# Kernel optimization log

Hardware: AMD Instinct MI355X
Metric: run time of the kernel (lower is better)

The kernel has to match this reference:

```python
import jax, jax.numpy as jnp
import numpy as np

# Dimensions (see shape_source)
B, L, D, H = 2, 2048, 768, 12   # batch, seq_len, hidden, heads (bert-base)
E, T, W = 32, 8, 4               # entities per doc, triggers = first T entities, span width
R, N = 57, 20                    # relation types, NOTA embeddings

# Static (trigger, object) pair index lists: s in [0,T), o in [0,E), s != o  -> P = T*(E-1)
_s = np.repeat(np.arange(T), E)
_o = np.tile(np.arange(E), T)
_keep = _s != _o
S_IDX = jnp.asarray(_s[_keep])   # [P]
O_IDX = jnp.asarray(_o[_keep])   # [P]
P = int(_keep.sum())             # 248


def setup_inputs() -> dict:
    key = jax.random.key(0)
    k1, k2, k3, k4, k5 = jax.random.split(key, 5)
    return {
        "sequence_output": jax.random.normal(k1, (B, L, D), jnp.float32),
        # attention weights are nonnegative (post-softmax) -> uniform fill
        "attention": jax.random.uniform(k2, (B, H, L, L), jnp.float32),
        "relation_embeddings": jax.random.normal(k3, (R, 3 * D), jnp.float32),
        "nota_embeddings": jax.random.normal(k4, (N, 3 * D), jnp.float32),
        "span_starts": jax.random.randint(k5, (B, E), 0, L - W, dtype=jnp.int32),
    }


def reference(sequence_output, attention, relation_embeddings, nota_embeddings, span_starts):
    # Span token indices: [B, E, W]
    idx = span_starts[..., None] + jnp.arange(W)
    b_ix = jnp.arange(B)[:, None, None]

    # Ragged span mean-pooling of token embeddings -> entity embeddings [B, E, D]
    ent_emb = sequence_output[b_ix, idx].mean(axis=2)

    # Mean over span tokens of attention rows -> per-entity attention [B, E, H, L]
    att_t = attention.transpose(0, 2, 1, 3)          # [B, L, H, L]
    ent_att = att_t[b_ix, idx].mean(axis=2)          # [B, E, H, L]

    # Localized context per (trigger s, object o) pair:
    # A = A_s * A_o ; q = sum over heads ; a = q / q.sum() ; c = H^T a
    A = ent_att[:, S_IDX] * ent_att[:, O_IDX]        # [B, P, H, L]
    q = A.sum(axis=2)                                 # [B, P, L]
    a = q / q.sum(axis=-1, keepdims=True)             # [B, P, L]
    c = jnp.einsum('bpl,bld->bpd', a, sequence_output)  # [B, P, D]

    # concat(e_s, e_o, c) -> [B, P, 3D]
    embs = jnp.concatenate([ent_emb[:, S_IDX], ent_emb[:, O_IDX], c], axis=-1)

    # Relation scoring against learned codebooks
    scores = embs @ relation_embeddings.T             # [B, P, R]
    nota_scores = (embs @ nota_embeddings.T).max(axis=-1, keepdims=True)  # [B, P, 1]
    return jnp.concatenate([nota_scores, scores], axis=-1)  # [B, P, R+1]
```

## Files before the change

kernel.cpp:

```cpp
#include <hip/hip_runtime.h>
#include <hip/hip_bf16.h>
#include <math.h>

#define BB 2
#define LL 2048
#define DD 768
#define HH 12
#define EE 32
#define RR 57
#define NN 20
#define PP 248
#define MM 256
#define KS 8
#define KCH (LL / KS)

#define ENT_EMB_OFF 0
#define A16_OFF   (BB * EE * DD)
#define A16_F     (BB * MM * LL / 2)
#define CPART_OFF (A16_OFF + A16_F)

#define PT4 4
#define NPT4 62

#define NQBLK (BB * 256)
#define NEBLK (EE * BB)
#define ASTRIDE 388

typedef __attribute__((ext_vector_type(8))) short bf16x8;
typedef __attribute__((ext_vector_type(4))) float f32x4;

__device__ __forceinline__ unsigned short f2bf(float f) {
    __hip_bfloat16 h = __float2bfloat16(f);
    return __builtin_bit_cast(unsigned short, h);
}
__device__ __forceinline__ float bf2f(unsigned short u) {
    unsigned int x = ((unsigned int)u) << 16;
    return __builtin_bit_cast(float, x);
}
__device__ __forceinline__ void pair_so(int p, int& s, int& o) {
    s = p / 31;
    int r = p - s * 31;
    o = (r < s) ? r : r + 1;
}
__device__ __forceinline__ float dot4(float4 a, float4 b) {
    return a.x * b.x + a.y * b.y + a.z * b.z + a.w * b.w;
}

__global__ __launch_bounds__(256) void kP(const float* __restrict__ seq,
                                          const float* __restrict__ att,
                                          const int* __restrict__ spans,
                                          float* __restrict__ ws) {
    __shared__ __align__(16) float att_s[8][ASTRIDE];
    __shared__ int sp_s[EE];
    int bid = blockIdx.x;
    int t = threadIdx.x;

    if (bid < NQBLK) {
        int xcd = bid & 7, i = bid >> 3;
        int chunk = xcd * (NQBLK / 8) + i;
        int b = chunk >> 8, l0 = (chunk & 255) * 8;
        if (t < EE) sp_s[t] = spans[b * EE + t];
        __syncthreads();
        for (int i2 = t; i2 < EE * HH * 2; i2 += 256) {
            int seg = i2 & 1, eh = i2 >> 1;
            int e = eh / HH, h = eh - e * HH;
            const float* base = att + ((size_t)(b * HH + h) * LL + sp_s[e]) * LL + l0 + seg * 4;
            float4 v0 = *(const float4*)base;
            float4 v1 = *(const float4*)(base + LL);
            float4 v2 = *(const float4*)(base + 2 * LL);
            float4 v3 = *(const float4*)(base + 3 * LL);
            att_s[seg * 4 + 0][eh] = 0.25f * (v0.x + v1.x + v2.x + v3.x);
            att_s[seg * 4 + 1][eh] = 0.25f * (v0.y + v1.y + v2.y + v3.y);
            att_s[seg * 4 + 2][eh] = 0.25f * (v0.z + v1.z + v2.z + v3.z);
            att_s[seg * 4 + 3][eh] = 0.25f * (v0.w + v1.w + v2.w + v3.w);
        }
        __syncthreads();
        int p = t, s, o;
        pair_so(p, s, o);
        float q[8];
        #pragma unroll
        for (int l = 0; l < 8; ++l) {
            float4 a0 = *(const float4*)&att_s[l][s * HH];
            float4 a1 = *(const float4*)&att_s[l][s * HH + 4];
            float4 a2 = *(const float4*)&att_s[l][s * HH + 8];
            float4 b0 = *(const float4*)&att_s[l][o * HH];
            float4 b1 = *(const float4*)&att_s[l][o * HH + 4];
            float4 b2 = *(const float4*)&att_s[l][o * HH + 8];
            q[l] = dot4(a0, b0) + dot4(a1, b1) + dot4(a2, b2);
        }
        unsigned short* A16 = (unsigned short*)(ws + A16_OFF) + (size_t)(b * MM + p) * LL + l0;
        #pragma unroll
        for (int i2 = 0; i2 < 2; ++i2) {
            ushort4 ov = make_ushort4(f2bf(q[i2 * 4 + 0]), f2bf(q[i2 * 4 + 1]),
                                      f2bf(q[i2 * 4 + 2]), f2bf(q[i2 * 4 + 3]));
            *(ushort4*)(A16 + i2 * 4) = ov;
        }
    } else {
        int bx = bid - NQBLK;
        int e = bx & 31, b = bx >> 5;
        int st = spans[b * EE + e];
        float* ee = ws + ENT_EMB_OFF + (size_t)(b * EE + e) * DD;
        const float* srow = seq + (size_t)(b * LL + st) * DD;
        for (int d = t; d < DD; d += 256) {
            ee[d] = 0.25f * (srow[d] + srow[DD + d] + srow[2 * DD + d] + srow[3 * DD + d]);
        }
    }
}

__global__ __launch_bounds__(256) void k3_gemm(const float* __restrict__ seq,
                                               float* __restrict__ ws) {
    int m0 = blockIdx.x * 64, n0 = blockIdx.y * 64;
    int ks = blockIdx.z & (KS - 1), b = blockIdx.z >> 3;
    const unsigned short* A = (const unsigned short*)(ws + A16_OFF) + (size_t)b * MM * LL;
    __shared__ __align__(16) short As[64][40];
    __shared__ __align__(16) short Bs[64][40];
    int t = threadIdx.x;
    int row = t >> 2, seg = t & 3;
    int bl = t >> 3, bd = t & 7;
    int w = t >> 6, lane = t & 63;
    int wr = w >> 1, wc = w & 1;
    int fr = lane & 15, kb = lane >> 4;
    f32x4 acc[2][2] = {};
    int k0c = ks * KCH;
    for (int st = 0; st < KCH / 32; ++st) {
        int kk = k0c + st * 32;
        *(uint4*)&As[row][seg * 8] = *(const uint4*)(A + (size_t)(m0 + row) * LL + kk + seg * 8);
        {
            const float* sp2 = seq + (size_t)(b * LL + kk + bl) * DD + n0 + bd * 8;
            float4 u0 = *(const float4*)sp2;
            float4 u1 = *(const float4*)(sp2 + 4);
            unsigned short bv[8] = {f2bf(u0.x), f2bf(u0.y), f2bf(u0.z), f2bf(u0.w),
                                    f2bf(u1.x), f2bf(u1.y), f2bf(u1.z), f2bf(u1.w)};
            #pragma unroll
            for (int i = 0; i < 8; ++i) {
                int k = (i + bd) & 7;
                Bs[bd * 8 + k][bl] = (short)bv[k];
            }
        }
        __syncthreads();
        bf16x8 af[2], bfr[2];
        #pragma unroll
        for (int i = 0; i < 2; ++i) af[i] = *(bf16x8*)&As[wr * 32 + i * 16 + fr][kb * 8];
        #pragma unroll
        for (int j = 0; j < 2; ++j) bfr[j] = *(bf16x8*)&Bs[wc * 32 + j * 16 + fr][kb * 8];
        #pragma unroll
        for (int i = 0; i < 2; ++i)
            #pragma unroll
            for (int j = 0; j < 2; ++j)
                acc[i][j] = __builtin_amdgcn_mfma_f32_16x16x32_bf16(af[i], bfr[j], acc[i][j], 0, 0, 0);
        __syncthreads();
    }
    float* cp = ws + CPART_OFF + (size_t)((ks * BB + b) * MM) * DD;
    #pragma unroll
    for (int i = 0; i < 2; ++i)
        #pragma unroll
        for (int j = 0; j < 2; ++j)
            #pragma unroll
            for (int r = 0; r < 4; ++r) {
                int gm = m0 + wr * 32 + i * 16 + kb * 4 + r;
                int gn = n0 + wc * 32 + j * 16 + fr;
                cp[(size_t)gm * DD + gn] = acc[i][j][r];
            }
}

__global__ __launch_bounds__(256, 1) void k4_score(const float* __restrict__ rel,
                                                   const float* __restrict__ nota,
                                                   const float* __restrict__ ws,
                                                   float* __restrict__ out) {
    int pt = blockIdx.x, b = blockIdx.y, gz = blockIdx.z;
    int tid = threadIdx.x, w = tid >> 6, lane = tid & 63;
    __shared__ float red_s[4][PT4];
    __shared__ float qs_s[PT4];
    __shared__ float nota_s[PT4][NN];
    {
        const unsigned short* A16 =
            (const unsigned short*)(ws + A16_OFF) + (size_t)(b * MM + pt * PT4) * LL;
        #pragma unroll
        for (int j = 0; j < PT4; ++j) {
            ushort4 u0 = *(const ushort4*)(A16 + (size_t)j * LL + tid * 8);
            ushort4 u1 = *(const ushort4*)(A16 + (size_t)j * LL + tid * 8 + 4);
            float v = bf2f(u0.x) + bf2f(u0.y) + bf2f(u0.z) + bf2f(u0.w)
                    + bf2f(u1.x) + bf2f(u1.y) + bf2f(u1.z) + bf2f(u1.w);
            #pragma unroll
            for (int off = 32; off > 0; off >>= 1) v += __shfl_xor(v, off, 64);
            if (lane == 0) red_s[w][j] = v;
        }
        __syncthreads();
        if (tid < PT4)
            qs_s[tid] = 1.0f / (red_s[0][tid] + red_s[1][tid] + red_s[2][tid] + red_s[3][tid]);
        __syncthreads();
    }
    float4 er[PT4][9];
    #pragma unroll
    for (int j = 0; j < PT4; ++j) {
        int p = pt * PT4 + j;
        int s, o;
        pair_so(p, s, o);
        const float4* es = (const float4*)(ws + ENT_EMB_OFF + (size_t)(b * EE + s) * DD);
        const float4* eo = (const float4*)(ws + ENT_EMB_OFF + (size_t)(b * EE + o) * DD);
        float qs = qs_s[j];
        #pragma unroll
        for (int i4 = 0; i4 < 3; ++i4) er[j][i4] = es[i4 * 64 + lane];
        #pragma unroll
        for (int i4 = 0; i4 < 3; ++i4) er[j][3 + i4] = eo[i4 * 64 + lane];
        #pragma unroll
        for (int i4 = 0; i4 < 3; ++i4) {
            float4 sum = make_float4(0.f, 0.f, 0.f, 0.f);
            #pragma unroll
            for (int ls = 0; ls < KS; ++ls) {
                const float4* cp = (const float4*)(ws + CPART_OFF +
                                   (size_t)((ls * BB + b) * MM + p) * DD);
                float4 v = cp[i4 * 64 + lane];
                sum.x += v.x; sum.y += v.y; sum.z += v.z; sum.w += v.w;
            }
            er[j][6 + i4] = make_float4(sum.x * qs, sum.y * qs, sum.z * qs, sum.w * qs);
        }
    }
    int lo = (gz == 0) ? 0 : 39;
    int hi = (gz == 0) ? 39 : (RR + NN);
    for (int base = lo + w * 2; base < hi; base += 8) {
        int r1 = base + 1;
        bool has1 = (r1 < hi);
        const float4* code0 = (base < RR)
            ? (const float4*)(rel + (size_t)base * 3 * DD)
            : (const float4*)(nota + (size_t)(base - RR) * 3 * DD);
        const float4* code1 = has1
            ? ((r1 < RR) ? (const float4*)(rel + (size_t)r1 * 3 * DD)
                         : (const float4*)(nota + (size_t)(r1 - RR) * 3 * DD))
            : code0;
        float acc0[PT4] = {0.f, 0.f, 0.f, 0.f};
        float acc1[PT4] = {0.f, 0.f, 0.f, 0.f};
        #pragma unroll
        for (int i4 = 0; i4 < 9; ++i4) {
            float4 c0 = code0[i4 * 64 + lane];
            float4 c1 = code1[i4 * 64 + lane];
            #pragma unroll
            for (int j = 0; j < PT4; ++j) {
                acc0[j] += dot4(c0, er[j][i4]);
                acc1[j] += dot4(c1, er[j][i4]);
            }
        }
        #pragma unroll
        for (int j = 0; j < PT4; ++j) {
            float v0 = acc0[j], v1 = acc1[j];
            #pragma unroll
            for (int off = 32; off > 0; off >>= 1) {
                v0 += __shfl_xor(v0, off, 64);
                v1 += __shfl_xor(v1, off, 64);
            }
            if (lane == 0) {
                int p = pt * PT4 + j;
                if (base < RR) out[(size_t)(b * PP + p) * (RR + 1) + 1 + base] = v0;
                else nota_s[j][base - RR] = v0;
                if (has1) {
                    if (r1 < RR) out[(size_t)(b * PP + p) * (RR + 1) + 1 + r1] = v1;
                    else nota_s[j][r1 - RR] = v1;
                }
            }
        }
    }
    __syncthreads();
    if (gz == 1 && tid < PT4) {
        float m = -INFINITY;
        #pragma unroll
        for (int n = 0; n < NN; ++n) m = fmaxf(m, nota_s[tid][n]);
        out[(size_t)(b * PP + pt * PT4 + tid) * (RR + 1)] = m;
    }
}

extern "C" void kernel_launch(void* const* d_in, const int* in_sizes, int n_in,
                              void* d_out, int out_size, void* d_ws, size_t ws_size,
                              hipStream_t stream) {
    const float* seq   = (const float*)d_in[0];
    const float* att   = (const float*)d_in[1];
    const float* rel   = (const float*)d_in[2];
    const float* nota  = (const float*)d_in[3];
    const int*   spans = (const int*)d_in[4];
    float* ws  = (float*)d_ws;
    float* out = (float*)d_out;

    kP<<<NQBLK + NEBLK, 256, 0, stream>>>(seq, att, spans, ws);
    k3_gemm<<<dim3(MM / 64, DD / 64, KS * BB), 256, 0, stream>>>(seq, ws);
    k4_score<<<dim3(NPT4, BB, 2), 256, 0, stream>>>(rel, nota, ws, out);
}
```

Measured before the change: 47.58 us.

## Fuse attention-pooling and split-K GEMM into one kernel with counter-based waits

The pooling kernel and the split-K GEMM are merged into one launch. Each GEMM block spins on a per-(batch, k-chunk) atomic counter until the 32 pooling blocks covering its K range have written their A rows, so GEMM work can overlap with the rest of pooling and one launch disappears. The split-K partial outputs are also stored as bf16 instead of fp32, which halves the write and reread traffic in the scoring kernel at some cost in precision. The spin-wait depends on the pooling blocks being scheduled before the GEMM blocks that wait on them, and the counters must be zeroed with an extra memset each call.

```diff
diff --git a/kernel.cpp b/kernel.cpp
--- a/kernel.cpp
+++ b/kernel.cpp
@@ -18,12 +18,15 @@
 #define A16_OFF   (BB * EE * DD)
 #define A16_F     (BB * MM * LL / 2)
 #define CPART_OFF (A16_OFF + A16_F)
+#define CPART_F16 (KS * BB * MM * DD / 2)
+#define CNT_OFF   (CPART_OFF + CPART_F16)
 
 #define PT4 4
 #define NPT4 62
 
 #define NQBLK (BB * 256)
 #define NEBLK (EE * BB)
+#define NGBLK 768
 #define ASTRIDE 388
 
 typedef __attribute__((ext_vector_type(8))) short bf16x8;
@@ -46,16 +49,18 @@
     return a.x * b.x + a.y * b.y + a.z * b.z + a.w * b.w;
 }
 
-__global__ __launch_bounds__(256) void kP(const float* __restrict__ seq,
-                                          const float* __restrict__ att,
-                                          const int* __restrict__ spans,
-                                          float* __restrict__ ws) {
-    __shared__ __align__(16) float att_s[8][ASTRIDE];
-    __shared__ int sp_s[EE];
+__global__ __launch_bounds__(256) void kPG(const float* __restrict__ seq,
+                                           const float* __restrict__ att,
+                                           const int* __restrict__ spans,
+                                           float* __restrict__ ws) {
+    __shared__ __align__(16) char smem[12544];
     int bid = blockIdx.x;
     int t = threadIdx.x;
+    int* cnt = (int*)(ws + CNT_OFF);
 
     if (bid < NQBLK) {
+        float (*att_s)[ASTRIDE] = (float (*)[ASTRIDE])smem;
+        int* sp_s = (int*)(smem + 8 * ASTRIDE * 4);
         int xcd = bid & 7, i = bid >> 3;
         int chunk = xcd * (NQBLK / 8) + i;
         int b = chunk >> 8, l0 = (chunk & 255) * 8;
@@ -95,7 +100,12 @@
                                       f2bf(q[i2 * 4 + 2]), f2bf(q[i2 * 4 + 3]));
             *(ushort4*)(A16 + i2 * 4) = ov;
         }
-    } else {
+        __syncthreads();
+        if (t == 0) {
+            __threadfence();
+            atomicAdd(&cnt[b * 8 + (l0 >> 8)], 1);
+        }
+    } else if (bid < NQBLK + NEBLK) {
         int bx = bid - NQBLK;
         int e = bx & 31, b = bx >> 5;
         int st = spans[b * EE + e];
@@ -104,63 +114,73 @@
         for (int d = t; d < DD; d += 256) {
             ee[d] = 0.25f * (srow[d] + srow[DD + d] + srow[2 * DD + d] + srow[3 * DD + d]);
         }
-    }
-}
-
-__global__ __launch_bounds__(256) void k3_gemm(const float* __restrict__ seq,
-                                               float* __restrict__ ws) {
-    int m0 = blockIdx.x * 64, n0 = blockIdx.y * 64;
-    int ks = blockIdx.z & (KS - 1), b = blockIdx.z >> 3;
-    const unsigned short* A = (const unsigned short*)(ws + A16_OFF) + (size_t)b * MM * LL;
-    __shared__ __align__(16) short As[64][40];
-    __shared__ __align__(16) short Bs[64][40];
-    int t = threadIdx.x;
-    int row = t >> 2, seg = t & 3;
-    int bl = t >> 3, bd = t & 7;
-    int w = t >> 6, lane = t & 63;
-    int wr = w >> 1, wc = w & 1;
-    int fr = lane & 15, kb = lane >> 4;
-    f32x4 acc[2][2] = {};
-    int k0c = ks * KCH;
-    for (int st = 0; st < KCH / 32; ++st) {
-        int kk = k0c + st * 32;
-        *(uint4*)&As[row][seg * 8] = *(const uint4*)(A + (size_t)(m0 + row) * LL + kk + seg * 8);
-        {
-            const float* sp2 = seq + (size_t)(b * LL + kk + bl) * DD + n0 + bd * 8;
-            float4 u0 = *(const float4*)sp2;
-            float4 u1 = *(const float4*)(sp2 + 4);
-            unsigned short bv[8] = {f2bf(u0.x), f2bf(u0.y), f2bf(u0.z), f2bf(u0.w),
-                                    f2bf(u1.x), f2bf(u1.y), f2bf(u1.z), f2bf(u1.w)};
-            #pragma unroll
-            for (int i = 0; i < 8; ++i) {
-                int k = (i + bd) & 7;
-                Bs[bd * 8 + k][bl] = (short)bv[k];
-            }
-        }
-        __syncthreads();
-        bf16x8 af[2], bfr[2];
-        #pragma unroll
-        for (int i = 0; i < 2; ++i) af[i] = *(bf16x8*)&As[wr * 32 + i * 16 + fr][kb * 8];
-        #pragma unroll
-        for (int j = 0; j < 2; ++j) bfr[j] = *(bf16x8*)&Bs[wc * 32 + j * 16 + fr][kb * 8];
+    } else {
+        short (*As)[40] = (short (*)[40])smem;
+        short (*Bs)[40] = (short (*)[40])(smem + 5120);
+        int g = bid - NQBLK - NEBLK;
+        int m0 = (g & 3) * 64;
+        int n0 = ((g >> 2) % 12) * 64;
+        int z = g / 48;
+        int ks = z & 7, b = z >> 3;
+        if (t == 0) {
+            while (__hip_atomic_load(&cnt[b * 8 + ks], __ATOMIC_RELAXED,
+                                     __HIP_MEMORY_SCOPE_AGENT) < 32)
+                __builtin_amdgcn_s_sleep(8);
+        }
+        __syncthreads();
+        __threadfence();
+        const unsigned short* A =
+            (const unsigned short*)(ws + A16_OFF) + (size_t)b * MM * LL;
+        int row = t >> 2, seg = t & 3;
+        int bl = t >> 3, bd = t & 7;
+        int w = t >> 6, lane = t & 63;
+        int wr = w >> 1, wc = w & 1;
+        int fr = lane & 15, kb = lane >> 4;
+        f32x4 acc[2][2] = {};
+        int k0c = ks * KCH;
+        for (int st = 0; st < KCH / 32; ++st) {
+            int kk = k0c + st * 32;
+            *(uint4*)&As[row][seg * 8] =
+                *(const uint4*)(A + (size_t)(m0 + row) * LL + kk + seg * 8);
+            {
+                const float* sp2 = seq + (size_t)(b * LL + kk + bl) * DD + n0 + bd * 8;
+                float4 u0 = *(const float4*)sp2;
+                float4 u1 = *(const float4*)(sp2 + 4);
+                unsigned short bv[8] = {f2bf(u0.x), f2bf(u0.y), f2bf(u0.z), f2bf(u0.w),
+                                        f2bf(u1.x), f2bf(u1.y), f2bf(u1.z), f2bf(u1.w)};
+                #pragma unroll
+                for (int i = 0; i < 8; ++i) {
+                    int k = (i + bd) & 7;
+                    Bs[bd * 8 + k][bl] = (short)bv[k];
+                }
+            }
+            __syncthreads();
+            bf16x8 af[2], bfr[2];
+            #pragma unroll
+            for (int i = 0; i < 2; ++i) af[i] = *(bf16x8*)&As[wr * 32 + i * 16 + fr][kb * 8];
+            #pragma unroll
+            for (int j = 0; j < 2; ++j) bfr[j] = *(bf16x8*)&Bs[wc * 32 + j * 16 + fr][kb * 8];
+            #pragma unroll
+            for (int i = 0; i < 2; ++i)
+                #pragma unroll
+                for (int j = 0; j < 2; ++j)
+                    acc[i][j] = __builtin_amdgcn_mfma_f32_16x16x32_bf16(
+                        af[i], bfr[j], acc[i][j], 0, 0, 0);
+            __syncthreads();
+        }
+        unsigned short* cp =
+            (unsigned short*)(ws + CPART_OFF) + (size_t)((ks * BB + b) * MM) * DD;
         #pragma unroll
         for (int i = 0; i < 2; ++i)
             #pragma unroll
             for (int j = 0; j < 2; ++j)
-                acc[i][j] = __builtin_amdgcn_mfma_f32_16x16x32_bf16(af[i], bfr[j], acc[i][j], 0, 0, 0);
-        __syncthreads();
-    }
-    float* cp = ws + CPART_OFF + (size_t)((ks * BB + b) * MM) * DD;
-    #pragma unroll
-    for (int i = 0; i < 2; ++i)
-        #pragma unroll
-        for (int j = 0; j < 2; ++j)
-            #pragma unroll
-            for (int r = 0; r < 4; ++r) {
-                int gm = m0 + wr * 32 + i * 16 + kb * 4 + r;
-                int gn = n0 + wc * 32 + j * 16 + fr;
-                cp[(size_t)gm * DD + gn] = acc[i][j][r];
-            }
+                #pragma unroll
+                for (int r = 0; r < 4; ++r) {
+                    int gm = m0 + wr * 32 + i * 16 + kb * 4 + r;
+                    int gn = n0 + wc * 32 + j * 16 + fr;
+                    cp[(size_t)gm * DD + gn] = f2bf(acc[i][j][r]);
+                }
+    }
 }
 
 __global__ __launch_bounds__(256, 1) void k4_score(const float* __restrict__ rel,
@@ -208,10 +228,11 @@
             float4 sum = make_float4(0.f, 0.f, 0.f, 0.f);
             #pragma unroll
             for (int ls = 0; ls < KS; ++ls) {
-                const float4* cp = (const float4*)(ws + CPART_OFF +
-                                   (size_t)((ls * BB + b) * MM + p) * DD);
-                float4 v = cp[i4 * 64 + lane];
-                sum.x += v.x; sum.y += v.y; sum.z += v.z; sum.w += v.w;
+                const unsigned short* cp = (const unsigned short*)(ws + CPART_OFF) +
+                                           (size_t)((ls * BB + b) * MM + p) * DD;
+                ushort4 v = *(const ushort4*)(cp + (i4 * 64 + lane) * 4);
+                sum.x += bf2f(v.x); sum.y += bf2f(v.y);
+                sum.z += bf2f(v.z); sum.w += bf2f(v.w);
             }
             er[j][6 + i4] = make_float4(sum.x * qs, sum.y * qs, sum.z * qs, sum.w * qs);
         }
@@ -279,7 +300,7 @@
     float* ws  = (float*)d_ws;
     float* out = (float*)d_out;
 
-    kP<<<NQBLK + NEBLK, 256, 0, stream>>>(seq, att, spans, ws);
-    k3_gemm<<<dim3(MM / 64, DD / 64, KS * BB), 256, 0, stream>>>(seq, ws);
+    hipMemsetAsync((char*)d_ws + (size_t)CNT_OFF * 4, 0, 16 * sizeof(int), stream);
+    kPG<<<NQBLK + NEBLK + NGBLK, 256, 0, stream>>>(seq, att, spans, ws);
     k4_score<<<dim3(NPT4, BB, 2), 256, 0, stream>>>(rel, nota, ws, out);
 }
```

Result: slower. 169.1 us (+255.4%).
